# Optimization experiments

Measured on AMD Instinct MI355X. Metric: run time of the kernel, lower is better.

The kernel has to match this reference:

```python
import jax, jax.numpy as jnp
import numpy as np


def _lstm(x, Wk, Wr, b, reverse, return_seq):
    # Keras LSTM with activation='relu', recurrent_activation='sigmoid'.
    # Wk: (F, 4H), Wr: (H, 4H), b: (4H). Gate order: i, f, c, o.
    if reverse:
        x = jnp.flip(x, 1)
    H = Wr.shape[0]
    xg = jnp.einsum('btf,fg->btg', x, Wk) + b  # (B, T, 4H)
    B = x.shape[0]

    def step(carry, g_t):
        h, c = carry
        g = g_t + h @ Wr
        i = jax.nn.sigmoid(g[:, :H])
        f = jax.nn.sigmoid(g[:, H:2 * H])
        cc = jax.nn.relu(g[:, 2 * H:3 * H])
        o = jax.nn.sigmoid(g[:, 3 * H:])
        c = f * c + i * cc
        h = o * jax.nn.relu(c)
        return (h, c), h

    init = (jnp.zeros((B, H), x.dtype), jnp.zeros((B, H), x.dtype))
    (h, _), hs = jax.lax.scan(step, init, jnp.swapaxes(xg, 0, 1))
    if return_seq:
        hs = jnp.swapaxes(hs, 0, 1)  # (B, T, H)
        if reverse:
            hs = jnp.flip(hs, 1)
        return hs
    return h


def setup_inputs() -> dict:
    key = jax.random.key(0)
    ks = jax.random.split(key, 24)
    B, LA, T, F = 256, 200, 512, 128
    s = 0.05
    d = {
        'inputA': jax.random.randint(ks[0], (B, LA), 0, 1000),
        'inputB': jax.random.normal(ks[1], (B, T, F), jnp.float32),
        'emb': jax.random.normal(ks[2], (1000, 3), jnp.float32) * s,
        'w1': jax.random.normal(ks[3], (600, 256), jnp.float32) * s,
        'b1': jnp.zeros((256,), jnp.float32),
        'w2': jax.random.normal(ks[4], (256, 128), jnp.float32) * s,
        'b2': jnp.zeros((128,), jnp.float32),
        'w3': jax.random.normal(ks[5], (128, 64), jnp.float32) * s,
        'b3': jnp.zeros((64,), jnp.float32),
        'k1f': jax.random.normal(ks[6], (128, 512), jnp.float32) * s,
        'r1f': jax.random.normal(ks[7], (128, 512), jnp.float32) * s,
        'bb1f': jnp.zeros((512,), jnp.float32),
        'k1b': jax.random.normal(ks[8], (128, 512), jnp.float32) * s,
        'r1b': jax.random.normal(ks[9], (128, 512), jnp.float32) * s,
        'bb1b': jnp.zeros((512,), jnp.float32),
        'k2f': jax.random.normal(ks[10], (256, 256), jnp.float32) * s,
        'r2f': jax.random.normal(ks[11], (64, 256), jnp.float32) * s,
        'bb2f': jnp.zeros((256,), jnp.float32),
        'k2b': jax.random.normal(ks[12], (256, 256), jnp.float32) * s,
        'r2b': jax.random.normal(ks[13], (64, 256), jnp.float32) * s,
        'bb2b': jnp.zeros((256,), jnp.float32),
        'wz1': jax.random.normal(ks[14], (192, 2), jnp.float32) * s,
        'bz1': jnp.zeros((2,), jnp.float32),
        'wz2': jax.random.normal(ks[15], (2, 1), jnp.float32) * s,
        'bz2': jnp.zeros((1,), jnp.float32),
        'wt1': jax.random.normal(ks[16], (192, 2), jnp.float32) * s,
        'bt1': jnp.zeros((2,), jnp.float32),
        'wt2': jax.random.normal(ks[17], (2, 1), jnp.float32) * s,
        'bt2': jnp.zeros((1,), jnp.float32),
    }
    return d


def reference(inputA, inputB, emb, w1, b1, w2, b2, w3, b3,
              k1f, r1f, bb1f, k1b, r1b, bb1b,
              k2f, r2f, bb2f, k2b, r2b, bb2b,
              wz1, bz1, wz2, bz2, wt1, bt1, wt2, bt2):
    B = inputA.shape[0]
    # Embedding branch
    x = emb[inputA]                       # (B, LA, 3)
    x = x.reshape(B, -1)                  # flatten -> (B, 600)
    x = jax.nn.relu(x @ w1 + b1)
    x = jax.nn.relu(x @ w2 + b2)
    x = jax.nn.relu(x @ w3 + b3)          # (B, 64)
    # BiLSTM branch
    y_f = _lstm(inputB, k1f, r1f, bb1f, reverse=False, return_seq=True)
    y_b = _lstm(inputB, k1b, r1b, bb1b, reverse=True, return_seq=True)
    y = jnp.concatenate([y_f, y_b], axis=-1)   # (B, T, 256)
    h_f = _lstm(y, k2f, r2f, bb2f, reverse=False, return_seq=False)
    h_b = _lstm(y, k2b, r2b, bb2b, reverse=True, return_seq=False)
    y = jnp.concatenate([h_f, h_b], axis=-1)    # (B, 128)
    combined = jnp.concatenate([x, y], axis=-1)  # (B, 192)
    z = jax.nn.relu(combined @ wz1 + bz1) @ wz2 + bz2
    t = jax.nn.relu(combined @ wt1 + bt1) @ wt2 + bt2
    return (z, t)
```

## Files before the change

kernel.cpp:

```cpp
#include <hip/hip_runtime.h>

typedef __attribute__((ext_vector_type(8))) short s8v;
typedef __attribute__((ext_vector_type(4))) short s4v;
typedef __attribute__((ext_vector_type(4))) float f4v;
typedef __attribute__((ext_vector_type(4))) unsigned u4v;

#if __has_builtin(__builtin_amdgcn_exp2f)
#define EXP2(x) __builtin_amdgcn_exp2f(x)
#else
#define EXP2(x) exp2f(x)
#endif
#if __has_builtin(__builtin_amdgcn_rcpf)
#define RCP(x) __builtin_amdgcn_rcpf(x)
#else
#define RCP(x) (1.0f/(x))
#endif

#define LOG2E 1.4426950408889634f

__device__ __forceinline__ short f2bf(float f) {
    union { float f; unsigned u; } x; x.f = f;
    unsigned r = (x.u + 0x7FFFu + ((x.u >> 16) & 1u)) >> 16;
    return (short)r;
}
__device__ __forceinline__ float bflo(unsigned u) {
    union { unsigned u; float f; } x; x.u = u << 16; return x.f;
}
__device__ __forceinline__ float bfhi(unsigned u) {
    union { unsigned u; float f; } x; x.u = u & 0xffff0000u; return x.f;
}
__device__ __forceinline__ unsigned cvt_pk_bf16(float lo, float hi) {
    unsigned r;
    asm("v_cvt_pk_bf16_f32 %0, %1, %2" : "=v"(r) : "v"(lo), "v"(hi));
    return r;
}
__device__ __forceinline__ void lds_barrier() {
    asm volatile("s_waitcnt lgkmcnt(0)\n\ts_barrier" ::: "memory");
}

__global__ __launch_bounds__(256) void prep_embed_kernel(
        const float* __restrict__ k1f, const float* __restrict__ r1f,
        const float* __restrict__ k1b, const float* __restrict__ r1b,
        const float* __restrict__ k2f, const float* __restrict__ r2f,
        const float* __restrict__ k2b, const float* __restrict__ r2b,
        short* __restrict__ WB1, short* __restrict__ WB2,
        const int* __restrict__ inputA, const float* __restrict__ emb,
        const float* __restrict__ w1, const float* __restrict__ b1,
        const float* __restrict__ w2, const float* __restrict__ b2,
        const float* __restrict__ w3, const float* __restrict__ b3,
        float* __restrict__ xe) {
    if (blockIdx.x < 1024) {
        int idx = blockIdx.x * 256 + threadIdx.x;
        if (idx < 262144) {
            int j = idx & 7, l = (idx >> 3) & 63, c = (idx >> 9) & 7, n = (idx >> 12) & 31, d = (idx >> 17) & 1;
            int coln = n * 16 + (l & 15);
            int k = c * 32 + ((l >> 4) * 8) + j;
            const float* Wk = d ? k1b : k1f;
            const float* Wr = d ? r1b : r1f;
            float v = (c < 4) ? Wk[k * 512 + coln] : Wr[(k - 128) * 512 + coln];
            float sc = ((n >> 3) == 2) ? 1.0f : -LOG2E;
            WB1[idx] = f2bf(v * sc);
        }
        if (idx < 163840) {
            int d = idx / 81920, r0 = idx % 81920;
            int n = r0 / 5120, r1 = r0 % 5120;
            int c = r1 / 512, li = r1 % 512;
            int l = li >> 3, j = li & 7;
            int coln = n * 16 + (l & 15);
            int k = c * 32 + ((l >> 4) * 8) + j;
            const float* Wk = d ? k2b : k2f;
            const float* Wr = d ? r2b : r2f;
            float v = (k < 256) ? Wk[k * 256 + coln] : Wr[(k - 256) * 256 + coln];
            float sc = ((n >> 2) == 2) ? 1.0f : -LOG2E;
            WB2[idx] = f2bf(v * sc);
        }
        return;
    }
    __shared__ float row[600];
    __shared__ float h1[256];
    __shared__ float h2[128];
    int b = blockIdx.x - 1024, t = threadIdx.x;
    if (t < 200) {
        int idx = inputA[b * 200 + t];
        row[t * 3 + 0] = emb[idx * 3 + 0];
        row[t * 3 + 1] = emb[idx * 3 + 1];
        row[t * 3 + 2] = emb[idx * 3 + 2];
    }
    __syncthreads();
    float a = b1[t];
    for (int k = 0; k < 600; k++) a += row[k] * w1[k * 256 + t];
    h1[t] = fmaxf(a, 0.f);
    __syncthreads();
    if (t < 128) {
        float a2 = b2[t];
        for (int k = 0; k < 256; k++) a2 += h1[k] * w2[k * 128 + t];
        h2[t] = fmaxf(a2, 0.f);
    }
    __syncthreads();
    if (t < 64) {
        float a3 = b3[t];
        for (int k = 0; k < 128; k++) a3 += h2[k] * w3[k * 64 + t];
        xe[b * 64 + t] = fmaxf(a3, 0.f);
    }
}

__global__ __launch_bounds__(512, 2) void megastep(
        const float* __restrict__ x, const short* __restrict__ WB1, const short* __restrict__ WB2,
        const float* __restrict__ bb1f, const float* __restrict__ bb1b,
        const float* __restrict__ bb2f, const float* __restrict__ bb2b,
        short* __restrict__ yfr, short* __restrict__ xgA, short* __restrict__ xgB,
        float* __restrict__ c1st, short* __restrict__ h1st,
        float* __restrict__ c2st, short* __restrict__ h2st,
        float* __restrict__ h2o, int k, int TC, int NC) {
    __shared__ short hA[2048];
    __shared__ short hB[2048];
    __shared__ __align__(16) short stg[38912];
    const int tid = threadIdx.x, lane = tid & 63, w = tid >> 6;
    const int bid = blockIdx.x;
    const int tgn = TC >> 3;

    if (bid < 32) {
        const int cl = k - 1;
        if (cl < 0 || cl >= NC) return;
        const int t0 = cl * TC;
        const int first = (cl == 0);
        const int btile = bid & 15, dir = bid >> 4;
        const int col = lane & 15, q = lane >> 4, u = (w << 4) + col;
        const int sb = dir * 16 + btile;

        s8v wf[4][4];
#pragma unroll
        for (int ti = 0; ti < 4; ti++)
#pragma unroll
            for (int c = 0; c < 4; c++)
                wf[ti][c] = *(const s8v*)(WB1 + ((((dir * 32 + (w + 8 * ti)) * 8) + 4 + c) * 64 + lane) * 8);

        float cst[4];
        if (first) {
#pragma unroll
            for (int r = 0; r < 4; r++) cst[r] = 0.f;
            for (int i = tid; i < 2048; i += 512) hA[i] = 0;
        } else {
            f4v cv = *(const f4v*)(c1st + ((size_t)sb * 8 + w) * 256 + lane * 4);
#pragma unroll
            for (int r = 0; r < 4; r++) cst[r] = cv[r];
            for (int i = tid; i < 2048; i += 512) hA[i] = h1st[sb * 2048 + i];
        }
        __syncthreads();

        const short* xgp = ((cl & 1) ? xgB : xgA) + (size_t)sb * TC * 8192 + w * 1024 + lane * 8;
        u4v pe0 = *(const u4v*)(xgp);
        u4v pe1 = *(const u4v*)(xgp + 512);
        u4v po0 = *(const u4v*)(xgp + 8192);
        u4v po1 = *(const u4v*)(xgp + 8192 + 512);

        const int hidx = (w >> 1) * 512 + ((u >> 3) & 3) * 128 + (u & 7);

        for (int s = 0; s < TC; s += 2) {
            {
                s8v ah[4];
#pragma unroll
                for (int cc = 0; cc < 4; cc++) ah[cc] = *(const s8v*)&hA[(cc * 64 + lane) * 8];
                if (w >= 4 && s > 0) {
                    int tp = t0 + s - 1;
                    if (dir) tp = 511 - tp;
                    s8v hv = (w == 4) ? ah[0] : (w == 5) ? ah[1] : (w == 6) ? ah[2] : ah[3];
                    *(s8v*)(yfr + (((size_t)(btile * 512 + tp) * 8) + dir * 4 + (w - 4)) * 512 + lane * 8) = hv;
                }
                f4v acc[4];
                acc[0][0] = bflo(pe0[0]); acc[0][1] = bfhi(pe0[0]); acc[0][2] = bflo(pe0[1]); acc[0][3] = bfhi(pe0[1]);
                acc[1][0] = bflo(pe0[2]); acc[1][1] = bfhi(pe0[2]); acc[1][2] = bflo(pe0[3]); acc[1][3] = bfhi(pe0[3]);
                acc[2][0] = bflo(pe1[0]); acc[2][1] = bfhi(pe1[0]); acc[2][2] = bflo(pe1[1]); acc[2][3] = bfhi(pe1[1]);
                acc[3][0] = bflo(pe1[2]); acc[3][1] = bfhi(pe1[2]); acc[3][2] = bflo(pe1[3]); acc[3][3] = bfhi(pe1[3]);
                {
                    const short* np = xgp + (size_t)(s + 2) * 8192;
                    pe0 = *(const u4v*)np;
                    pe1 = *(const u4v*)(np + 512);
                }
#pragma unroll
                for (int cc = 0; cc < 4; cc++)
#pragma unroll
                    for (int ti = 0; ti < 4; ti++)
                        acc[ti] = __builtin_amdgcn_mfma_f32_16x16x32_bf16(ah[cc], wf[ti][cc], acc[ti], 0, 0, 0);
                float hv_[4];
#pragma unroll
                for (int r = 0; r < 4; r++) {
                    float Ei = EXP2(acc[0][r]);
                    float Ef = EXP2(acc[1][r]);
                    float Eo = EXP2(acc[3][r]);
                    float rv = fmaxf(acc[2][r], 0.f);
                    float di = 1.f + Ei, df = 1.f + Ef;
                    float cn = fmaf(cst[r], di, rv * df) * RCP(di * df);
                    cst[r] = cn;
                    hv_[r] = fmaxf(cn, 0.f) * RCP(1.f + Eo);
                }
                unsigned p01 = cvt_pk_bf16(hv_[0], hv_[1]);
                unsigned p23 = cvt_pk_bf16(hv_[2], hv_[3]);
                short* hb = &hB[hidx + (q << 5)];
                hb[0]  = (short)p01;  hb[8]  = (short)(p01 >> 16);
                hb[16] = (short)p23;  hb[24] = (short)(p23 >> 16);
                lds_barrier();
            }
            {
                s8v ah[4];
#pragma unroll
                for (int cc = 0; cc < 4; cc++) ah[cc] = *(const s8v*)&hB[(cc * 64 + lane) * 8];
                if (w >= 4) {
                    int tp = t0 + s;
                    if (dir) tp = 511 - tp;
                    s8v hv = (w == 4) ? ah[0] : (w == 5) ? ah[1] : (w == 6) ? ah[2] : ah[3];
                    *(s8v*)(yfr + (((size_t)(btile * 512 + tp) * 8) + dir * 4 + (w - 4)) * 512 + lane * 8) = hv;
                }
                f4v acc[4];
                acc[0][0] = bflo(po0[0]); acc[0][1] = bfhi(po0[0]); acc[0][2] = bflo(po0[1]); acc[0][3] = bfhi(po0[1]);
                acc[1][0] = bflo(po0[2]); acc[1][1] = bfhi(po0[2]); acc[1][2] = bflo(po0[3]); acc[1][3] = bfhi(po0[3]);
                acc[2][0] = bflo(po1[0]); acc[2][1] = bfhi(po1[0]); acc[2][2] = bflo(po1[1]); acc[2][3] = bfhi(po1[1]);
                acc[3][0] = bflo(po1[2]); acc[3][1] = bfhi(po1[2]); acc[3][2] = bflo(po1[3]); acc[3][3] = bfhi(po1[3]);
                {
                    const short* np = xgp + (size_t)(s + 3) * 8192;
                    po0 = *(const u4v*)np;
                    po1 = *(const u4v*)(np + 512);
                }
#pragma unroll
                for (int cc = 0; cc < 4; cc++)
#pragma unroll
                    for (int ti = 0; ti < 4; ti++)
                        acc[ti] = __builtin_amdgcn_mfma_f32_16x16x32_bf16(ah[cc], wf[ti][cc], acc[ti], 0, 0, 0);
                float hv_[4];
#pragma unroll
                for (int r = 0; r < 4; r++) {
                    float Ei = EXP2(acc[0][r]);
                    float Ef = EXP2(acc[1][r]);
                    float Eo = EXP2(acc[3][r]);
                    float rv = fmaxf(acc[2][r], 0.f);
                    float di = 1.f + Ei, df = 1.f + Ef;
                    float cn = fmaf(cst[r], di, rv * df) * RCP(di * df);
                    cst[r] = cn;
                    hv_[r] = fmaxf(cn, 0.f) * RCP(1.f + Eo);
                }
                unsigned p01 = cvt_pk_bf16(hv_[0], hv_[1]);
                unsigned p23 = cvt_pk_bf16(hv_[2], hv_[3]);
                short* hb = &hA[hidx + (q << 5)];
                hb[0]  = (short)p01;  hb[8]  = (short)(p01 >> 16);
                hb[16] = (short)p23;  hb[24] = (short)(p23 >> 16);
                lds_barrier();
            }
        }
        if (w >= 4) {
            int tp = t0 + TC - 1;
            if (dir) tp = 511 - tp;
            s8v hv = *(const s8v*)&hA[((w - 4) * 64 + lane) * 8];
            *(s8v*)(yfr + (((size_t)(btile * 512 + tp) * 8) + dir * 4 + (w - 4)) * 512 + lane * 8) = hv;
        }
        f4v cv;
#pragma unroll
        for (int r = 0; r < 4; r++) cv[r] = cst[r];
        *(f4v*)(c1st + ((size_t)sb * 8 + w) * 256 + lane * 4) = cv;
        for (int i = tid; i < 2048; i += 512) h1st[sb * 2048 + i] = hA[i];
        return;
    }

    if (bid < 64) {
        const int c2 = k - 2;
        if (c2 < 0 || c2 >= NC) return;
        const int first = (c2 == 0), last = (c2 == NC - 1);
        const int btile = (bid - 32) & 15, dir = (bid - 32) >> 4;
        const int b0 = btile << 4;
        const int w4 = w & 3;
        const int col = lane & 15, q = lane >> 4, u = (w4 << 4) + col;
        const int sb = dir * 16 + btile;
        const int t0 = c2 * TC;
        float* ring = (float*)stg;

        float cst[4], hl[4] = {0.f, 0.f, 0.f, 0.f};
        if (first) {
#pragma unroll
            for (int r = 0; r < 4; r++) cst[r] = 0.f;
            for (int i = tid; i < 1024; i += 512) hA[i] = 0;
        } else {
            f4v cv = *(const f4v*)(c2st + ((size_t)sb * 4 + w4) * 256 + lane * 4);
#pragma unroll
            for (int r = 0; r < 4; r++) cst[r] = cv[r];
            for (int i = tid; i < 1024; i += 512) hA[i] = h2st[sb * 1024 + i];
        }
        __syncthreads();

        const int hidx = (w4 >> 1) * 512 + ((u >> 3) & 3) * 128 + (u & 7);

        if (w < 4) {
            s8v wr_[4][2];
#pragma unroll
            for (int ti = 0; ti < 4; ti++)
#pragma unroll
                for (int cc = 0; cc < 2; cc++)
                    wr_[ti][cc] = *(const s8v*)(WB2 + ((((dir * 16 + (w4 + 4 * ti)) * 10) + 8 + cc) * 64 + lane) * 8);
            lds_barrier();
            for (int s = 0; s < TC; s += 2) {
                {
                    s8v ah[2];
#pragma unroll
                    for (int cc = 0; cc < 2; cc++) ah[cc] = *(const s8v*)&hA[(cc * 64 + lane) * 8];
                    f4v acc[4];
                    const int slot = s & 3;
#pragma unroll
                    for (int ti = 0; ti < 4; ti++)
                        acc[ti] = *(const f4v*)&ring[(((slot * 4 + w4) * 4 + ti) * 64 + lane) * 4];
#pragma unroll
                    for (int cc = 0; cc < 2; cc++)
#pragma unroll
                        for (int ti = 0; ti < 4; ti++)
                            acc[ti] = __builtin_amdgcn_mfma_f32_16x16x32_bf16(ah[cc], wr_[ti][cc], acc[ti], 0, 0, 0);
#pragma unroll
                    for (int r = 0; r < 4; r++) {
                        float Ei = EXP2(acc[0][r]);
                        float Ef = EXP2(acc[1][r]);
                        float Eo = EXP2(acc[3][r]);
                        float rv = fmaxf(acc[2][r], 0.f);
                        float di = 1.f + Ei, df = 1.f + Ef;
                        float cn = fmaf(cst[r], di, rv * df) * RCP(di * df);
                        cst[r] = cn;
                        hl[r] = fmaxf(cn, 0.f) * RCP(1.f + Eo);
                    }
                    unsigned p01 = cvt_pk_bf16(hl[0], hl[1]);
                    unsigned p23 = cvt_pk_bf16(hl[2], hl[3]);
                    short* hb = &hB[hidx + (q << 5)];
                    hb[0]  = (short)p01;  hb[8]  = (short)(p01 >> 16);
                    hb[16] = (short)p23;  hb[24] = (short)(p23 >> 16);
                    lds_barrier();
                }
                {
                    s8v ah[2];
#pragma unroll
                    for (int cc = 0; cc < 2; cc++) ah[cc] = *(const s8v*)&hB[(cc * 64 + lane) * 8];
                    f4v acc[4];
                    const int slot = (s + 1) & 3;
#pragma unroll
                    for (int ti = 0; ti < 4; ti++)
                        acc[ti] = *(const f4v*)&ring[(((slot * 4 + w4) * 4 + ti) * 64 + lane) * 4];
#pragma unroll
                    for (int cc = 0; cc < 2; cc++)
#pragma unroll
                        for (int ti = 0; ti < 4; ti++)
                            acc[ti] = __builtin_amdgcn_mfma_f32_16x16x32_bf16(ah[cc], wr_[ti][cc], acc[ti], 0, 0, 0);
#pragma unroll
                    for (int r = 0; r < 4; r++) {
                        float Ei = EXP2(acc[0][r]);
                        float Ef = EXP2(acc[1][r]);
                        float Eo = EXP2(acc[3][r]);
                        float rv = fmaxf(acc[2][r], 0.f);
                        float di = 1.f + Ei, df = 1.f + Ef;
                        float cn = fmaf(cst[r], di, rv * df) * RCP(di * df);
                        cst[r] = cn;
                        hl[r] = fmaxf(cn, 0.f) * RCP(1.f + Eo);
                    }
                    unsigned p01 = cvt_pk_bf16(hl[0], hl[1]);
                    unsigned p23 = cvt_pk_bf16(hl[2], hl[3]);
                    short* hb = &hA[hidx + (q << 5)];
                    hb[0]  = (short)p01;  hb[8]  = (short)(p01 >> 16);
                    hb[16] = (short)p23;  hb[24] = (short)(p23 >> 16);
                    lds_barrier();
                }
            }
            f4v cv;
#pragma unroll
            for (int r = 0; r < 4; r++) cv[r] = cst[r];
            *(f4v*)(c2st + ((size_t)sb * 4 + w4) * 256 + lane * 4) = cv;
        } else {
            const int p4 = w - 4;
            s8v wk[4][8];
#pragma unroll
            for (int ti = 0; ti < 4; ti++)
#pragma unroll
                for (int c = 0; c < 8; c++)
                    wk[ti][c] = *(const s8v*)(WB2 + ((((dir * 16 + (p4 + 4 * ti)) * 10) + c) * 64 + lane) * 8);
            const float* bb = dir ? bb2b : bb2f;
            float bias[4];
#pragma unroll
            for (int ti = 0; ti < 4; ti++) {
                const int tile = p4 + 4 * ti;
                float sc = ((tile >> 2) == 2) ? 1.0f : -LOG2E;
                bias[ti] = sc * bb[tile * 16 + (lane & 15)];
            }
            int tg0 = dir ? (511 - t0) : t0;
            const short* yrd = yfr + ((size_t)(btile * 512 + tg0) * 8) * 512 + lane * 8;
            const int ystep = dir ? -4096 : 4096;
            s8v aE[8], aO[8];
#pragma unroll
            for (int pt = 0; pt < 2; pt++) {
                s8v a[8];
#pragma unroll
                for (int c = 0; c < 8; c++) a[c] = *(const s8v*)(yrd + c * 512);
                yrd += ystep;
                f4v acc[4];
#pragma unroll
                for (int ti = 0; ti < 4; ti++) { f4v z = {bias[ti], bias[ti], bias[ti], bias[ti]}; acc[ti] = z; }
#pragma unroll
                for (int c = 0; c < 8; c++)
#pragma unroll
                    for (int ti = 0; ti < 4; ti++)
                        acc[ti] = __builtin_amdgcn_mfma_f32_16x16x32_bf16(a[c], wk[ti][c], acc[ti], 0, 0, 0);
#pragma unroll
                for (int ti = 0; ti < 4; ti++)
                    *(f4v*)&ring[(((pt * 4 + p4) * 4 + ti) * 64 + lane) * 4] = acc[ti];
            }
#pragma unroll
            for (int c = 0; c < 8; c++) aE[c] = *(const s8v*)(yrd + c * 512);
            yrd += ystep;
#pragma unroll
            for (int c = 0; c < 8; c++) aO[c] = *(const s8v*)(yrd + c * 512);
            yrd += ystep;
            lds_barrier();
            for (int s = 0; s < TC; s += 2) {
                {
                    const int t = s + 2;
                    if (t < TC) {
                        f4v acc[4];
#pragma unroll
                        for (int ti = 0; ti < 4; ti++) { f4v z = {bias[ti], bias[ti], bias[ti], bias[ti]}; acc[ti] = z; }
#pragma unroll
                        for (int c = 0; c < 8; c++)
#pragma unroll
                            for (int ti = 0; ti < 4; ti++)
                                acc[ti] = __builtin_amdgcn_mfma_f32_16x16x32_bf16(aE[c], wk[ti][c], acc[ti], 0, 0, 0);
                        const int slot = t & 3;
#pragma unroll
                        for (int ti = 0; ti < 4; ti++)
                            *(f4v*)&ring[(((slot * 4 + p4) * 4 + ti) * 64 + lane) * 4] = acc[ti];
                    }
                    if (s + 4 < TC) {
#pragma unroll
                        for (int c = 0; c < 8; c++) aE[c] = *(const s8v*)(yrd + c * 512);
                        yrd += ystep;
                    }
                    lds_barrier();
                }
                {
                    const int t = s + 3;
                    if (t < TC) {
                        f4v acc[4];
#pragma unroll
                        for (int ti = 0; ti < 4; ti++) { f4v z = {bias[ti], bias[ti], bias[ti], bias[ti]}; acc[ti] = z; }
#pragma unroll
                        for (int c = 0; c < 8; c++)
#pragma unroll
                            for (int ti = 0; ti < 4; ti++)
                                acc[ti] = __builtin_amdgcn_mfma_f32_16x16x32_bf16(aO[c], wk[ti][c], acc[ti], 0, 0, 0);
                        const int slot = t & 3;
#pragma unroll
                        for (int ti = 0; ti < 4; ti++)
                            *(f4v*)&ring[(((slot * 4 + p4) * 4 + ti) * 64 + lane) * 4] = acc[ti];
                    }
                    if (s + 5 < TC) {
#pragma unroll
                        for (int c = 0; c < 8; c++) aO[c] = *(const s8v*)(yrd + c * 512);
                        yrd += ystep;
                    }
                    lds_barrier();
                }
            }
        }
        __syncthreads();
        for (int i = tid; i < 1024; i += 512) h2st[sb * 1024 + i] = hA[i];
        if (last && w < 4) {
#pragma unroll
            for (int r = 0; r < 4; r++)
                h2o[((dir * 256) + b0 + q * 4 + r) * 64 + u] = hl[r];
        }
        return;
    }

    {
        const int cg = k;
        if (cg >= NC) return;
        const int t0 = cg * TC;
        const int g = bid - 64;
        const int btile = g & 15;
        const int rest = g >> 4;
        const int tg = rest % tgn;
        const int dir = rest / tgn;
        const int b0 = btile << 4;
        short* xg_w = (cg & 1) ? xgB : xgA;
        const int lane_ = lane;
        {
            int tglob = t0 + tg * 8 + w;
            if (dir) tglob = 511 - tglob;
            const int half = lane_ >> 5;
            const int f0 = (lane_ & 31) * 4;
            const int cx = f0 >> 5, qq = (f0 >> 3) & 3, j0 = f0 & 7;
#pragma unroll
            for (int rr = 0; rr < 8; rr++) {
                const int m = rr * 2 + half;
                const float* xp = x + ((size_t)(b0 + m) * 512 + tglob) * 128 + f0;
                f4v v4 = *(const f4v*)xp;
                const int slot = (qq << 4) | ((m ^ qq ^ (cx << 1)) & 15);
                s4v pk;
#pragma unroll
                for (int j = 0; j < 4; j++) pk[j] = f2bf(v4[j]);
                *(s4v*)&stg[(((w * 4 + cx) * 64 + slot) * 8) + j0] = pk;
            }
        }
        s8v wf[4][4];
#pragma unroll
        for (int ti = 0; ti < 4; ti++)
#pragma unroll
            for (int c = 0; c < 4; c++)
                wf[ti][c] = *(const s8v*)(WB1 + ((((dir * 32 + (w + 8 * ti)) * 8) + c) * 64 + lane) * 8);
        const float* bb = dir ? bb1b : bb1f;
        float bias[4];
#pragma unroll
        for (int ti = 0; ti < 4; ti++) {
            const int tile = w + 8 * ti;
            float sc = ((tile >> 3) == 2) ? 1.0f : -LOG2E;
            bias[ti] = sc * bb[tile * 16 + (lane & 15)];
        }
        __syncthreads();
        const size_t sb = dir * 16 + btile;
#pragma unroll 2
        for (int sl = 0; sl < 8; sl++) {
            s8v a[4];
#pragma unroll
            for (int c = 0; c < 4; c++) {
                const int slot = lane ^ (lane >> 4) ^ (c << 1);
                a[c] = *(const s8v*)&stg[((sl * 4 + c) * 64 + slot) * 8];
            }
            f4v acc[4];
#pragma unroll
            for (int ti = 0; ti < 4; ti++) { f4v z = {0.f, 0.f, 0.f, 0.f}; acc[ti] = z; }
#pragma unroll
            for (int c = 0; c < 4; c++)
#pragma unroll
                for (int ti = 0; ti < 4; ti++)
                    acc[ti] = __builtin_amdgcn_mfma_f32_16x16x32_bf16(a[c], wf[ti][c], acc[ti], 0, 0, 0);
            short* outp = xg_w + ((sb * TC + (size_t)(tg * 8 + sl)) * 8 + w) * 1024 + lane * 8;
#pragma unroll
            for (int p = 0; p < 2; p++) {
                s8v v;
#pragma unroll
                for (int j = 0; j < 4; j++) {
                    v[j]     = f2bf(acc[2 * p][j]     + bias[2 * p]);
                    v[4 + j] = f2bf(acc[2 * p + 1][j] + bias[2 * p + 1]);
                }
                *(s8v*)(outp + p * 512) = v;
            }
        }
    }
}

__global__ void heads_kernel(const float* __restrict__ xe, const float* __restrict__ h2o,
                             const float* __restrict__ wz1, const float* __restrict__ bz1,
                             const float* __restrict__ wz2, const float* __restrict__ bz2,
                             const float* __restrict__ wt1, const float* __restrict__ bt1,
                             const float* __restrict__ wt2, const float* __restrict__ bt2,
                             float* __restrict__ out) {
    int b = threadIdx.x;
    float cz0 = bz1[0], cz1 = bz1[1], ct0 = bt1[0], ct1 = bt1[1];
    for (int k = 0; k < 192; k++) {
        float v = (k < 64) ? xe[b * 64 + k]
                : (k < 128) ? h2o[b * 64 + (k - 64)]
                            : h2o[(256 + b) * 64 + (k - 128)];
        cz0 += v * wz1[k * 2 + 0];
        cz1 += v * wz1[k * 2 + 1];
        ct0 += v * wt1[k * 2 + 0];
        ct1 += v * wt1[k * 2 + 1];
    }
    cz0 = fmaxf(cz0, 0.f); cz1 = fmaxf(cz1, 0.f);
    ct0 = fmaxf(ct0, 0.f); ct1 = fmaxf(ct1, 0.f);
    out[b] = cz0 * wz2[0] + cz1 * wz2[1] + bz2[0];
    out[256 + b] = ct0 * wt2[0] + ct1 * wt2[1] + bt2[0];
}

extern "C" void kernel_launch(void* const* d_in, const int* in_sizes, int n_in,
                              void* d_out, int out_size, void* d_ws, size_t ws_size,
                              hipStream_t stream) {
    const int*   inputA = (const int*)d_in[0];
    const float* inputB = (const float*)d_in[1];
    const float* emb = (const float*)d_in[2];
    const float* w1  = (const float*)d_in[3];
    const float* b1  = (const float*)d_in[4];
    const float* w2  = (const float*)d_in[5];
    const float* b2  = (const float*)d_in[6];
    const float* w3  = (const float*)d_in[7];
    const float* b3  = (const float*)d_in[8];
    const float* k1f = (const float*)d_in[9];
    const float* r1f = (const float*)d_in[10];
    const float* bb1f= (const float*)d_in[11];
    const float* k1b = (const float*)d_in[12];
    const float* r1b = (const float*)d_in[13];
    const float* bb1b= (const float*)d_in[14];
    const float* k2f = (const float*)d_in[15];
    const float* r2f = (const float*)d_in[16];
    const float* bb2f= (const float*)d_in[17];
    const float* k2b = (const float*)d_in[18];
    const float* r2b = (const float*)d_in[19];
    const float* bb2b= (const float*)d_in[20];
    const float* wz1 = (const float*)d_in[21];
    const float* bz1 = (const float*)d_in[22];
    const float* wz2 = (const float*)d_in[23];
    const float* bz2 = (const float*)d_in[24];
    const float* wt1 = (const float*)d_in[25];
    const float* bt1 = (const float*)d_in[26];
    const float* wt2 = (const float*)d_in[27];
    const float* bt2 = (const float*)d_in[28];

    char* ws = (char*)d_ws;
    short* WB1  = (short*)(ws);
    short* WB2  = (short*)(ws + 524288);
    float* xe   = (float*)(ws + 851968);
    float* h2o  = (float*)(ws + 917504);
    float* c1st = (float*)(ws + 1048576);
    short* h1st = (short*)(ws + 1310720);
    float* c2st = (float*)(ws + 1441792);
    short* h2st = (short*)(ws + 1572864);
    short* yfr  = (short*)(ws + 2097152);
    float* out  = (float*)d_out;

    int TC = 32;
    if (69206016ull + 2ull * 64 * 524288 + 2ull * 64 * 262144 + 65536 <= ws_size) TC = 64;
    const int NC = 512 / TC;
    short* xgA = (short*)(ws + 69206016);
    short* xgB = xgA + (size_t)TC * 262144;
    const int grid = 64 + 4 * TC;

    prep_embed_kernel<<<1280, 256, 0, stream>>>(k1f, r1f, k1b, r1b, k2f, r2f, k2b, r2b,
                                                WB1, WB2, inputA, emb, w1, b1, w2, b2, w3, b3, xe);
    for (int k = 0; k < NC + 2; k++) {
        megastep<<<grid, 512, 0, stream>>>(inputB, WB1, WB2, bb1f, bb1b, bb2f, bb2b,
                                           yfr, xgA, xgB,
                                           c1st, h1st, c2st, h2st, h2o, k, TC, NC);
    }
    heads_kernel<<<1, 256, 0, stream>>>(xe, h2o, wz1, bz1, wz2, bz2, wt1, bt1, wt2, bt2, out);
}
```

Measured before the change: 686.8 us.

## Move layer-2 input projection into separate parallel blocks and batch embedding MLP

The layer-2 LSTM input projection (y @ Wk2) was computed by half the warps of each recurrent block through an LDS ring, in lockstep with the serial recurrence. It now runs in its own set of grid blocks one chunk ahead, writing bf16 gate preactivations to new double-buffered ygA/ygB buffers. The recurrent blocks then only load them, as layer 1 already does, and the pipeline gains one extra launch stage. Separately, the embedding MLP processes 8 batch rows per block to reuse weight loads, the yfr store is moved after the MFMAs, and TC is fixed at 32.

```diff
diff --git a/kernel.cpp b/kernel.cpp
--- a/kernel.cpp
+++ b/kernel.cpp
@@ -76,31 +76,72 @@
         }
         return;
     }
-    __shared__ float row[600];
-    __shared__ float h1[256];
-    __shared__ float h2[128];
-    int b = blockIdx.x - 1024, t = threadIdx.x;
-    if (t < 200) {
-        int idx = inputA[b * 200 + t];
-        row[t * 3 + 0] = emb[idx * 3 + 0];
-        row[t * 3 + 1] = emb[idx * 3 + 1];
-        row[t * 3 + 2] = emb[idx * 3 + 2];
+    __shared__ __align__(16) float row2[600][8];
+    __shared__ __align__(16) float h1r[256][8];
+    __shared__ __align__(16) float h2r[128][8];
+    int blk = blockIdx.x - 1024;
+    int b0 = blk * 8;
+    int t = threadIdx.x;
+    for (int i = t; i < 1600; i += 256) {
+        int r = i / 200, p = i - r * 200;
+        int idx = inputA[(b0 + r) * 200 + p];
+        row2[p * 3 + 0][r] = emb[idx * 3 + 0];
+        row2[p * 3 + 1][r] = emb[idx * 3 + 1];
+        row2[p * 3 + 2][r] = emb[idx * 3 + 2];
     }
     __syncthreads();
-    float a = b1[t];
-    for (int k = 0; k < 600; k++) a += row[k] * w1[k * 256 + t];
-    h1[t] = fmaxf(a, 0.f);
+    {
+        float acc[8];
+        float bv = b1[t];
+#pragma unroll
+        for (int r = 0; r < 8; r++) acc[r] = bv;
+        for (int k = 0; k < 600; k++) {
+            float wv = w1[k * 256 + t];
+            const f4v* rp = (const f4v*)&row2[k][0];
+            f4v r0 = rp[0], r1 = rp[1];
+#pragma unroll
+            for (int r = 0; r < 4; r++) acc[r] = fmaf(r0[r], wv, acc[r]);
+#pragma unroll
+            for (int r = 0; r < 4; r++) acc[4 + r] = fmaf(r1[r], wv, acc[4 + r]);
+        }
+#pragma unroll
+        for (int r = 0; r < 8; r++) h1r[t][r] = fmaxf(acc[r], 0.f);
+    }
     __syncthreads();
     if (t < 128) {
-        float a2 = b2[t];
-        for (int k = 0; k < 256; k++) a2 += h1[k] * w2[k * 128 + t];
-        h2[t] = fmaxf(a2, 0.f);
+        float acc[8];
+        float bv = b2[t];
+#pragma unroll
+        for (int r = 0; r < 8; r++) acc[r] = bv;
+        for (int k = 0; k < 256; k++) {
+            float wv = w2[k * 128 + t];
+            const f4v* rp = (const f4v*)&h1r[k][0];
+            f4v r0 = rp[0], r1 = rp[1];
+#pragma unroll
+            for (int r = 0; r < 4; r++) acc[r] = fmaf(r0[r], wv, acc[r]);
+#pragma unroll
+            for (int r = 0; r < 4; r++) acc[4 + r] = fmaf(r1[r], wv, acc[4 + r]);
+        }
+#pragma unroll
+        for (int r = 0; r < 8; r++) h2r[t][r] = fmaxf(acc[r], 0.f);
     }
     __syncthreads();
     if (t < 64) {
-        float a3 = b3[t];
-        for (int k = 0; k < 128; k++) a3 += h2[k] * w3[k * 64 + t];
-        xe[b * 64 + t] = fmaxf(a3, 0.f);
+        float acc[8];
+        float bv = b3[t];
+#pragma unroll
+        for (int r = 0; r < 8; r++) acc[r] = bv;
+        for (int k = 0; k < 128; k++) {
+            float wv = w3[k * 64 + t];
+            const f4v* rp = (const f4v*)&h2r[k][0];
+            f4v r0 = rp[0], r1 = rp[1];
+#pragma unroll
+            for (int r = 0; r < 4; r++) acc[r] = fmaf(r0[r], wv, acc[r]);
+#pragma unroll
+            for (int r = 0; r < 4; r++) acc[4 + r] = fmaf(r1[r], wv, acc[4 + r]);
+        }
+#pragma unroll
+        for (int r = 0; r < 8; r++) xe[(b0 + r) * 64 + t] = fmaxf(acc[r], 0.f);
     }
 }
 
@@ -109,6 +150,7 @@
         const float* __restrict__ bb1f, const float* __restrict__ bb1b,
         const float* __restrict__ bb2f, const float* __restrict__ bb2b,
         short* __restrict__ yfr, short* __restrict__ xgA, short* __restrict__ xgB,
+        short* __restrict__ ygA, short* __restrict__ ygB,
         float* __restrict__ c1st, short* __restrict__ h1st,
         float* __restrict__ c2st, short* __restrict__ h2st,
         float* __restrict__ h2o, int k, int TC, int NC) {
@@ -161,12 +203,6 @@
                 s8v ah[4];
 #pragma unroll
                 for (int cc = 0; cc < 4; cc++) ah[cc] = *(const s8v*)&hA[(cc * 64 + lane) * 8];
-                if (w >= 4 && s > 0) {
-                    int tp = t0 + s - 1;
-                    if (dir) tp = 511 - tp;
-                    s8v hv = (w == 4) ? ah[0] : (w == 5) ? ah[1] : (w == 6) ? ah[2] : ah[3];
-                    *(s8v*)(yfr + (((size_t)(btile * 512 + tp) * 8) + dir * 4 + (w - 4)) * 512 + lane * 8) = hv;
-                }
                 f4v acc[4];
                 acc[0][0] = bflo(pe0[0]); acc[0][1] = bfhi(pe0[0]); acc[0][2] = bflo(pe0[1]); acc[0][3] = bfhi(pe0[1]);
                 acc[1][0] = bflo(pe0[2]); acc[1][1] = bfhi(pe0[2]); acc[1][2] = bflo(pe0[3]); acc[1][3] = bfhi(pe0[3]);
@@ -182,6 +218,12 @@
 #pragma unroll
                     for (int ti = 0; ti < 4; ti++)
                         acc[ti] = __builtin_amdgcn_mfma_f32_16x16x32_bf16(ah[cc], wf[ti][cc], acc[ti], 0, 0, 0);
+                if (w >= 4 && s > 0) {
+                    int tp = t0 + s - 1;
+                    if (dir) tp = 511 - tp;
+                    s8v hv = (w == 4) ? ah[0] : (w == 5) ? ah[1] : (w == 6) ? ah[2] : ah[3];
+                    *(s8v*)(yfr + (((size_t)(btile * 512 + tp) * 8) + dir * 4 + (w - 4)) * 512 + lane * 8) = hv;
+                }
                 float hv_[4];
 #pragma unroll
                 for (int r = 0; r < 4; r++) {
@@ -205,12 +247,6 @@
                 s8v ah[4];
 #pragma unroll
                 for (int cc = 0; cc < 4; cc++) ah[cc] = *(const s8v*)&hB[(cc * 64 + lane) * 8];
-                if (w >= 4) {
-                    int tp = t0 + s;
-                    if (dir) tp = 511 - tp;
-                    s8v hv = (w == 4) ? ah[0] : (w == 5) ? ah[1] : (w == 6) ? ah[2] : ah[3];
-                    *(s8v*)(yfr + (((size_t)(btile * 512 + tp) * 8) + dir * 4 + (w - 4)) * 512 + lane * 8) = hv;
-                }
                 f4v acc[4];
                 acc[0][0] = bflo(po0[0]); acc[0][1] = bfhi(po0[0]); acc[0][2] = bflo(po0[1]); acc[0][3] = bfhi(po0[1]);
                 acc[1][0] = bflo(po0[2]); acc[1][1] = bfhi(po0[2]); acc[1][2] = bflo(po0[3]); acc[1][3] = bfhi(po0[3]);
@@ -226,6 +262,12 @@
 #pragma unroll
                     for (int ti = 0; ti < 4; ti++)
                         acc[ti] = __builtin_amdgcn_mfma_f32_16x16x32_bf16(ah[cc], wf[ti][cc], acc[ti], 0, 0, 0);
+                if (w >= 4) {
+                    int tp = t0 + s;
+                    if (dir) tp = 511 - tp;
+                    s8v hv = (w == 4) ? ah[0] : (w == 5) ? ah[1] : (w == 6) ? ah[2] : ah[3];
+                    *(s8v*)(yfr + (((size_t)(btile * 512 + tp) * 8) + dir * 4 + (w - 4)) * 512 + lane * 8) = hv;
+                }
                 float hv_[4];
 #pragma unroll
                 for (int r = 0; r < 4; r++) {
@@ -261,7 +303,7 @@
     }
 
     if (bid < 64) {
-        const int c2 = k - 2;
+        const int c2 = k - 3;
         if (c2 < 0 || c2 >= NC) return;
         const int first = (c2 == 0), last = (c2 == NC - 1);
         const int btile = (bid - 32) & 15, dir = (bid - 32) >> 4;
@@ -269,8 +311,13 @@
         const int w4 = w & 3;
         const int col = lane & 15, q = lane >> 4, u = (w4 << 4) + col;
         const int sb = dir * 16 + btile;
-        const int t0 = c2 * TC;
-        float* ring = (float*)stg;
+
+        s8v wf[4][2];
+#pragma unroll
+        for (int ti = 0; ti < 4; ti++)
+#pragma unroll
+            for (int c = 0; c < 2; c++)
+                wf[ti][c] = *(const s8v*)(WB2 + ((((dir * 16 + (w4 + 4 * ti)) * 10) + 8 + c) * 64 + lane) * 8);
 
         float cst[4], hl[4] = {0.f, 0.f, 0.f, 0.f};
         if (first) {
@@ -285,179 +332,97 @@
         }
         __syncthreads();
 
+        const short* ygp = ((c2 & 1) ? ygB : ygA) + (size_t)sb * TC * 4096 + w4 * 1024 + lane * 8;
+        u4v pe0, pe1, po0, po1;
+        if (w < 4) {
+            pe0 = *(const u4v*)(ygp);
+            pe1 = *(const u4v*)(ygp + 512);
+            po0 = *(const u4v*)(ygp + 4096);
+            po1 = *(const u4v*)(ygp + 4096 + 512);
+        }
         const int hidx = (w4 >> 1) * 512 + ((u >> 3) & 3) * 128 + (u & 7);
 
+        for (int s = 0; s < TC; s += 2) {
+            if (w < 4) {
+                s8v ah[2];
+#pragma unroll
+                for (int cc = 0; cc < 2; cc++) ah[cc] = *(const s8v*)&hA[(cc * 64 + lane) * 8];
+                f4v acc[4];
+                acc[0][0] = bflo(pe0[0]); acc[0][1] = bfhi(pe0[0]); acc[0][2] = bflo(pe0[1]); acc[0][3] = bfhi(pe0[1]);
+                acc[1][0] = bflo(pe0[2]); acc[1][1] = bfhi(pe0[2]); acc[1][2] = bflo(pe0[3]); acc[1][3] = bfhi(pe0[3]);
+                acc[2][0] = bflo(pe1[0]); acc[2][1] = bfhi(pe1[0]); acc[2][2] = bflo(pe1[1]); acc[2][3] = bfhi(pe1[1]);
+                acc[3][0] = bflo(pe1[2]); acc[3][1] = bfhi(pe1[2]); acc[3][2] = bflo(pe1[3]); acc[3][3] = bfhi(pe1[3]);
+                {
+                    const short* np = ygp + (size_t)(s + 2) * 4096;
+                    pe0 = *(const u4v*)np;
+                    pe1 = *(const u4v*)(np + 512);
+                }
+#pragma unroll
+                for (int cc = 0; cc < 2; cc++)
+#pragma unroll
+                    for (int ti = 0; ti < 4; ti++)
+                        acc[ti] = __builtin_amdgcn_mfma_f32_16x16x32_bf16(ah[cc], wf[ti][cc], acc[ti], 0, 0, 0);
+#pragma unroll
+                for (int r = 0; r < 4; r++) {
+                    float Ei = EXP2(acc[0][r]);
+                    float Ef = EXP2(acc[1][r]);
+                    float Eo = EXP2(acc[3][r]);
+                    float rv = fmaxf(acc[2][r], 0.f);
+                    float di = 1.f + Ei, df = 1.f + Ef;
+                    float cn = fmaf(cst[r], di, rv * df) * RCP(di * df);
+                    cst[r] = cn;
+                    hl[r] = fmaxf(cn, 0.f) * RCP(1.f + Eo);
+                }
+                unsigned p01 = cvt_pk_bf16(hl[0], hl[1]);
+                unsigned p23 = cvt_pk_bf16(hl[2], hl[3]);
+                short* hb = &hB[hidx + (q << 5)];
+                hb[0]  = (short)p01;  hb[8]  = (short)(p01 >> 16);
+                hb[16] = (short)p23;  hb[24] = (short)(p23 >> 16);
+            }
+            lds_barrier();
+            if (w < 4) {
+                s8v ah[2];
+#pragma unroll
+                for (int cc = 0; cc < 2; cc++) ah[cc] = *(const s8v*)&hB[(cc * 64 + lane) * 8];
+                f4v acc[4];
+                acc[0][0] = bflo(po0[0]); acc[0][1] = bfhi(po0[0]); acc[0][2] = bflo(po0[1]); acc[0][3] = bfhi(po0[1]);
+                acc[1][0] = bflo(po0[2]); acc[1][1] = bfhi(po0[2]); acc[1][2] = bflo(po0[3]); acc[1][3] = bfhi(po0[3]);
+                acc[2][0] = bflo(po1[0]); acc[2][1] = bfhi(po1[0]); acc[2][2] = bflo(po1[1]); acc[2][3] = bfhi(po1[1]);
+                acc[3][0] = bflo(po1[2]); acc[3][1] = bfhi(po1[2]); acc[3][2] = bflo(po1[3]); acc[3][3] = bfhi(po1[3]);
+                {
+                    const short* np = ygp + (size_t)(s + 3) * 4096;
+                    po0 = *(const u4v*)np;
+                    po1 = *(const u4v*)(np + 512);
+                }
+#pragma unroll
+                for (int cc = 0; cc < 2; cc++)
+#pragma unroll
+                    for (int ti = 0; ti < 4; ti++)
+                        acc[ti] = __builtin_amdgcn_mfma_f32_16x16x32_bf16(ah[cc], wf[ti][cc], acc[ti], 0, 0, 0);
+#pragma unroll
+                for (int r = 0; r < 4; r++) {
+                    float Ei = EXP2(acc[0][r]);
+                    float Ef = EXP2(acc[1][r]);
+                    float Eo = EXP2(acc[3][r]);
+                    float rv = fmaxf(acc[2][r], 0.f);
+                    float di = 1.f + Ei, df = 1.f + Ef;
+                    float cn = fmaf(cst[r], di, rv * df) * RCP(di * df);
+                    cst[r] = cn;
+                    hl[r] = fmaxf(cn, 0.f) * RCP(1.f + Eo);
+                }
+                unsigned p01 = cvt_pk_bf16(hl[0], hl[1]);
+                unsigned p23 = cvt_pk_bf16(hl[2], hl[3]);
+                short* hb = &hA[hidx + (q << 5)];
+                hb[0]  = (short)p01;  hb[8]  = (short)(p01 >> 16);
+                hb[16] = (short)p23;  hb[24] = (short)(p23 >> 16);
+            }
+            lds_barrier();
+        }
         if (w < 4) {
-            s8v wr_[4][2];
-#pragma unroll
-            for (int ti = 0; ti < 4; ti++)
-#pragma unroll
-                for (int cc = 0; cc < 2; cc++)
-                    wr_[ti][cc] = *(const s8v*)(WB2 + ((((dir * 16 + (w4 + 4 * ti)) * 10) + 8 + cc) * 64 + lane) * 8);
-            lds_barrier();
-            for (int s = 0; s < TC; s += 2) {
-                {
-                    s8v ah[2];
-#pragma unroll
-                    for (int cc = 0; cc < 2; cc++) ah[cc] = *(const s8v*)&hA[(cc * 64 + lane) * 8];
-                    f4v acc[4];
-                    const int slot = s & 3;
-#pragma unroll
-                    for (int ti = 0; ti < 4; ti++)
-                        acc[ti] = *(const f4v*)&ring[(((slot * 4 + w4) * 4 + ti) * 64 + lane) * 4];
-#pragma unroll
-                    for (int cc = 0; cc < 2; cc++)
-#pragma unroll
-                        for (int ti = 0; ti < 4; ti++)
-                            acc[ti] = __builtin_amdgcn_mfma_f32_16x16x32_bf16(ah[cc], wr_[ti][cc], acc[ti], 0, 0, 0);
-#pragma unroll
-                    for (int r = 0; r < 4; r++) {
-                        float Ei = EXP2(acc[0][r]);
-                        float Ef = EXP2(acc[1][r]);
-                        float Eo = EXP2(acc[3][r]);
-                        float rv = fmaxf(acc[2][r], 0.f);
-                        float di = 1.f + Ei, df = 1.f + Ef;
-                        float cn = fmaf(cst[r], di, rv * df) * RCP(di * df);
-                        cst[r] = cn;
-                        hl[r] = fmaxf(cn, 0.f) * RCP(1.f + Eo);
-                    }
-                    unsigned p01 = cvt_pk_bf16(hl[0], hl[1]);
-                    unsigned p23 = cvt_pk_bf16(hl[2], hl[3]);
-                    short* hb = &hB[hidx + (q << 5)];
-                    hb[0]  = (short)p01;  hb[8]  = (short)(p01 >> 16);
-                    hb[16] = (short)p23;  hb[24] = (short)(p23 >> 16);
-                    lds_barrier();
-                }
-                {
-                    s8v ah[2];
-#pragma unroll
-                    for (int cc = 0; cc < 2; cc++) ah[cc] = *(const s8v*)&hB[(cc * 64 + lane) * 8];
-                    f4v acc[4];
-                    const int slot = (s + 1) & 3;
-#pragma unroll
-                    for (int ti = 0; ti < 4; ti++)
-                        acc[ti] = *(const f4v*)&ring[(((slot * 4 + w4) * 4 + ti) * 64 + lane) * 4];
-#pragma unroll
-                    for (int cc = 0; cc < 2; cc++)
-#pragma unroll
-                        for (int ti = 0; ti < 4; ti++)
-                            acc[ti] = __builtin_amdgcn_mfma_f32_16x16x32_bf16(ah[cc], wr_[ti][cc], acc[ti], 0, 0, 0);
-#pragma unroll
-                    for (int r = 0; r < 4; r++) {
-                        float Ei = EXP2(acc[0][r]);
-                        float Ef = EXP2(acc[1][r]);
-                        float Eo = EXP2(acc[3][r]);
-                        float rv = fmaxf(acc[2][r], 0.f);
-                        float di = 1.f + Ei, df = 1.f + Ef;
-                        float cn = fmaf(cst[r], di, rv * df) * RCP(di * df);
-                        cst[r] = cn;
-                        hl[r] = fmaxf(cn, 0.f) * RCP(1.f + Eo);
-                    }
-                    unsigned p01 = cvt_pk_bf16(hl[0], hl[1]);
-                    unsigned p23 = cvt_pk_bf16(hl[2], hl[3]);
-                    short* hb = &hA[hidx + (q << 5)];
-                    hb[0]  = (short)p01;  hb[8]  = (short)(p01 >> 16);
-                    hb[16] = (short)p23;  hb[24] = (short)(p23 >> 16);
-                    lds_barrier();
-                }
-            }
             f4v cv;
 #pragma unroll
             for (int r = 0; r < 4; r++) cv[r] = cst[r];
             *(f4v*)(c2st + ((size_t)sb * 4 + w4) * 256 + lane * 4) = cv;
-        } else {
-            const int p4 = w - 4;
-            s8v wk[4][8];
-#pragma unroll
-            for (int ti = 0; ti < 4; ti++)
-#pragma unroll
-                for (int c = 0; c < 8; c++)
-                    wk[ti][c] = *(const s8v*)(WB2 + ((((dir * 16 + (p4 + 4 * ti)) * 10) + c) * 64 + lane) * 8);
-            const float* bb = dir ? bb2b : bb2f;
-            float bias[4];
-#pragma unroll
-            for (int ti = 0; ti < 4; ti++) {
-                const int tile = p4 + 4 * ti;
-                float sc = ((tile >> 2) == 2) ? 1.0f : -LOG2E;
-                bias[ti] = sc * bb[tile * 16 + (lane & 15)];
-            }
-            int tg0 = dir ? (511 - t0) : t0;
-            const short* yrd = yfr + ((size_t)(btile * 512 + tg0) * 8) * 512 + lane * 8;
-            const int ystep = dir ? -4096 : 4096;
-            s8v aE[8], aO[8];
-#pragma unroll
-            for (int pt = 0; pt < 2; pt++) {
-                s8v a[8];
-#pragma unroll
-                for (int c = 0; c < 8; c++) a[c] = *(const s8v*)(yrd + c * 512);
-                yrd += ystep;
-                f4v acc[4];
-#pragma unroll
-                for (int ti = 0; ti < 4; ti++) { f4v z = {bias[ti], bias[ti], bias[ti], bias[ti]}; acc[ti] = z; }
-#pragma unroll
-                for (int c = 0; c < 8; c++)
-#pragma unroll
-                    for (int ti = 0; ti < 4; ti++)
-                        acc[ti] = __builtin_amdgcn_mfma_f32_16x16x32_bf16(a[c], wk[ti][c], acc[ti], 0, 0, 0);
-#pragma unroll
-                for (int ti = 0; ti < 4; ti++)
-                    *(f4v*)&ring[(((pt * 4 + p4) * 4 + ti) * 64 + lane) * 4] = acc[ti];
-            }
-#pragma unroll
-            for (int c = 0; c < 8; c++) aE[c] = *(const s8v*)(yrd + c * 512);
-            yrd += ystep;
-#pragma unroll
-            for (int c = 0; c < 8; c++) aO[c] = *(const s8v*)(yrd + c * 512);
-            yrd += ystep;
-            lds_barrier();
-            for (int s = 0; s < TC; s += 2) {
-                {
-                    const int t = s + 2;
-                    if (t < TC) {
-                        f4v acc[4];
-#pragma unroll
-                        for (int ti = 0; ti < 4; ti++) { f4v z = {bias[ti], bias[ti], bias[ti], bias[ti]}; acc[ti] = z; }
-#pragma unroll
-                        for (int c = 0; c < 8; c++)
-#pragma unroll
-                            for (int ti = 0; ti < 4; ti++)
-                                acc[ti] = __builtin_amdgcn_mfma_f32_16x16x32_bf16(aE[c], wk[ti][c], acc[ti], 0, 0, 0);
-                        const int slot = t & 3;
-#pragma unroll
-                        for (int ti = 0; ti < 4; ti++)
-                            *(f4v*)&ring[(((slot * 4 + p4) * 4 + ti) * 64 + lane) * 4] = acc[ti];
-                    }
-                    if (s + 4 < TC) {
-#pragma unroll
-                        for (int c = 0; c < 8; c++) aE[c] = *(const s8v*)(yrd + c * 512);
-                        yrd += ystep;
-                    }
-                    lds_barrier();
-                }
-                {
-                    const int t = s + 3;
-                    if (t < TC) {
-                        f4v acc[4];
-#pragma unroll
-                        for (int ti = 0; ti < 4; ti++) { f4v z = {bias[ti], bias[ti], bias[ti], bias[ti]}; acc[ti] = z; }
-#pragma unroll
-                        for (int c = 0; c < 8; c++)
-#pragma unroll
-                            for (int ti = 0; ti < 4; ti++)
-                                acc[ti] = __builtin_amdgcn_mfma_f32_16x16x32_bf16(aO[c], wk[ti][c], acc[ti], 0, 0, 0);
-                        const int slot = t & 3;
-#pragma unroll
-                        for (int ti = 0; ti < 4; ti++)
-                            *(f4v*)&ring[(((slot * 4 + p4) * 4 + ti) * 64 + lane) * 4] = acc[ti];
-                    }
-                    if (s + 5 < TC) {
-#pragma unroll
-                        for (int c = 0; c < 8; c++) aO[c] = *(const s8v*)(yrd + c * 512);
-                        yrd += ystep;
-                    }
-                    lds_barrier();
-                }
-            }
         }
         __syncthreads();
         for (int i = tid; i < 1024; i += 512) h2st[sb * 1024 + i] = hA[i];
@@ -469,7 +434,7 @@
         return;
     }
 
-    {
+    if (bid < 64 + 4 * TC) {
         const int cg = k;
         if (cg >= NC) return;
         const int t0 = cg * TC;
@@ -480,12 +445,11 @@
         const int dir = rest / tgn;
         const int b0 = btile << 4;
         short* xg_w = (cg & 1) ? xgB : xgA;
-        const int lane_ = lane;
         {
             int tglob = t0 + tg * 8 + w;
             if (dir) tglob = 511 - tglob;
-            const int half = lane_ >> 5;
-            const int f0 = (lane_ & 31) * 4;
+            const int half = lane >> 5;
+            const int f0 = (lane & 31) * 4;
             const int cx = f0 >> 5, qq = (f0 >> 3) & 3, j0 = f0 & 7;
 #pragma unroll
             for (int rr = 0; rr < 8; rr++) {
@@ -532,6 +496,64 @@
                 for (int ti = 0; ti < 4; ti++)
                     acc[ti] = __builtin_amdgcn_mfma_f32_16x16x32_bf16(a[c], wf[ti][c], acc[ti], 0, 0, 0);
             short* outp = xg_w + ((sb * TC + (size_t)(tg * 8 + sl)) * 8 + w) * 1024 + lane * 8;
+#pragma unroll
+            for (int p = 0; p < 2; p++) {
+                s8v v;
+#pragma unroll
+                for (int j = 0; j < 4; j++) {
+                    v[j]     = f2bf(acc[2 * p][j]     + bias[2 * p]);
+                    v[4 + j] = f2bf(acc[2 * p + 1][j] + bias[2 * p + 1]);
+                }
+                *(s8v*)(outp + p * 512) = v;
+            }
+        }
+        return;
+    }
+
+    {
+        const int cg = k - 2;
+        if (cg < 0 || cg >= NC) return;
+        const int t0 = cg * TC;
+        const int g = bid - 64 - 4 * TC;
+        const int btile = g & 15;
+        const int rest = g >> 4;
+        const int tg = rest % tgn;
+        const int dir = rest / tgn;
+        short* yg_w = (cg & 1) ? ygB : ygA;
+        const int w4 = w & 3, sh = (w >> 2) * 4;
+        s8v wf[4][8];
+#pragma unroll
+        for (int ti = 0; ti < 4; ti++)
+#pragma unroll
+            for (int c = 0; c < 8; c++)
+                wf[ti][c] = *(const s8v*)(WB2 + ((((dir * 16 + (w4 + 4 * ti)) * 10) + c) * 64 + lane) * 8);
+        const float* bb = dir ? bb2b : bb2f;
+        float bias[4];
+#pragma unroll
+        for (int ti = 0; ti < 4; ti++) {
+            const int tile = w4 + 4 * ti;
+            float sc = ((tile >> 2) == 2) ? 1.0f : -LOG2E;
+            bias[ti] = sc * bb[tile * 16 + (lane & 15)];
+        }
+        const size_t sb = dir * 16 + btile;
+#pragma unroll
+        for (int si = 0; si < 4; si++) {
+            const int sl = sh + si;
+            int tglob = t0 + tg * 8 + sl;
+            if (dir) tglob = 511 - tglob;
+            s8v a[8];
+#pragma unroll
+            for (int c = 0; c < 8; c++)
+                a[c] = *(const s8v*)(yfr + (((size_t)(btile * 512 + tglob) * 8) + c) * 512 + lane * 8);
+            f4v acc[4];
+#pragma unroll
+            for (int ti = 0; ti < 4; ti++) { f4v z = {0.f, 0.f, 0.f, 0.f}; acc[ti] = z; }
+#pragma unroll
+            for (int c = 0; c < 8; c++)
+#pragma unroll
+                for (int ti = 0; ti < 4; ti++)
+                    acc[ti] = __builtin_amdgcn_mfma_f32_16x16x32_bf16(a[c], wf[ti][c], acc[ti], 0, 0, 0);
+            short* outp = yg_w + ((sb * TC + (size_t)(tg * 8 + sl)) * 4 + w4) * 1024 + lane * 8;
 #pragma unroll
             for (int p = 0; p < 2; p++) {
                 s8v v;
@@ -614,18 +636,19 @@
     short* yfr  = (short*)(ws + 2097152);
     float* out  = (float*)d_out;
 
-    int TC = 32;
-    if (69206016ull + 2ull * 64 * 524288 + 2ull * 64 * 262144 + 65536 <= ws_size) TC = 64;
+    const int TC = 32;
     const int NC = 512 / TC;
     short* xgA = (short*)(ws + 69206016);
     short* xgB = xgA + (size_t)TC * 262144;
-    const int grid = 64 + 4 * TC;
-
-    prep_embed_kernel<<<1280, 256, 0, stream>>>(k1f, r1f, k1b, r1b, k2f, r2f, k2b, r2b,
+    short* ygA = xgB + (size_t)TC * 262144;
+    short* ygB = ygA + (size_t)TC * 131072;
+    const int grid = 64 + 8 * TC;
+
+    prep_embed_kernel<<<1056, 256, 0, stream>>>(k1f, r1f, k1b, r1b, k2f, r2f, k2b, r2b,
                                                 WB1, WB2, inputA, emb, w1, b1, w2, b2, w3, b3, xe);
-    for (int k = 0; k < NC + 2; k++) {
+    for (int k = 0; k < NC + 3; k++) {
         megastep<<<grid, 512, 0, stream>>>(inputB, WB1, WB2, bb1f, bb1b, bb2f, bb2b,
-                                           yfr, xgA, xgB,
+                                           yfr, xgA, xgB, ygA, ygB,
                                            c1st, h1st, c2st, h2st, h2o, k, TC, NC);
     }
     heads_kernel<<<1, 256, 0, stream>>>(xe, h2o, wz1, bz1, wz2, bz2, wt1, bt1, wt2, bt2, out);
```

New measurement: 681.8 us. Within noise of the previous version (-0.7%).
